# Performance work log

Hardware: AMD Instinct MI355X
Metric: run time of the kernel (lower is better)

## Reference

```python
import jax, jax.numpy as jnp
import numpy as np

jax.config.update("jax_enable_x64", True)  # faithful int64 fixed-point requantize

B, K, N = 2048, 4096, 8192
INT32_MAX_MINUS = 2147418112  # threshold from multiply_by_quantize_mul


def setup_inputs() -> dict:
    key = jax.random.key(0)
    k1, k2, k3 = jax.random.split(key, 3)
    x = jax.random.randint(k1, (B, K), -128, 128, dtype=jnp.int8)
    weights = jax.random.randint(k2, (N, K), -128, 128, dtype=jnp.int8)
    bias = jax.random.randint(k3, (N, 1), -1024, 1024, dtype=jnp.int32)
    return {
        "x": x,
        "weights": weights,
        "bias": bias,
        "q_mantissa": 1431655765,   # ~2/3 in Q31 fixed point
        "exponent": -3,
        "output_zero_point": -5,
    }


def multiply_by_quantize_mul(x, q_mantissa, exponent):
    # Python precedence in original: (q_mantissa + (1<<15)) >> 16
    reduced_mantissa = ((q_mantissa + (1 << 15)) >> 16) if q_mantissa < INT32_MAX_MINUS else 32767
    total_shifts = 15 - exponent
    x = x * np.int64(reduced_mantissa)
    x = x + np.int64(1 << (total_shifts - 1))  # rounding term
    return jnp.right_shift(x, total_shifts)    # arithmetic shift on signed int64


def reference(x, weights, bias, q_mantissa, exponent, output_zero_point):
    # int8 GEMM accumulated in int32: result[b, n] = sum_k x[b, k] * w[n, k]
    acc = jnp.einsum("bk,nk->bn", x.astype(jnp.int32), weights.astype(jnp.int32))
    acc = acc + bias.T  # bias [N,1] -> [1,N], broadcast over batch
    acc = multiply_by_quantize_mul(acc.astype(jnp.int64), q_mantissa, exponent)
    acc = acc + np.int64(output_zero_point)
    out = jnp.clip(acc, -128, 127).astype(jnp.int8)
    return out
```

## Files before the change

kernel.cpp:

```cpp
#include <hip/hip_runtime.h>

#define DEVI __device__ __forceinline__

typedef int i32x4  __attribute__((ext_vector_type(4)));
typedef int i32x16 __attribute__((ext_vector_type(16)));

static constexpr int Bdim = 2048;
static constexpr int Kdim = 4096;
static constexpr int Ndim = 8192;
static constexpr int BK   = 64;
static constexpr int NT   = Kdim / BK;

typedef __attribute__((address_space(1))) const unsigned int gas_t;
typedef __attribute__((address_space(3))) unsigned int las_t;

DEVI void gload_lds16(const void* g, void* l) {
    __builtin_amdgcn_global_load_lds((gas_t*)g, (las_t*)l, 16, 0, 0);
}

DEVI int pack4(i32x4 v) {
    return (v[0] & 255) | ((v[1] & 255) << 8) | ((v[2] & 255) << 16) | (v[3] << 24);
}

__global__ void pack_i32_to_i8(const int* __restrict__ in, char* __restrict__ out, int n16) {
    int i = blockIdx.x * blockDim.x + threadIdx.x;
    if (i >= n16) return;
    const i32x4* src = (const i32x4*)in + (size_t)i * 4;
    i32x4 r;
    r[0] = pack4(src[0]);
    r[1] = pack4(src[1]);
    r[2] = pack4(src[2]);
    r[3] = pack4(src[3]);
    ((i32x4*)out)[i] = r;
}

__global__ __launch_bounds__(512, 4)
void gemm2b(const char* __restrict__ A8, const char* __restrict__ B8,
            const int* __restrict__ bias,
            const int* __restrict__ qm_p, const int* __restrict__ ex_p,
            const int* __restrict__ zp_p, int* __restrict__ out) {
    __shared__ __align__(16) char smem[49152];

    const int tid  = threadIdx.x;
    const int wid  = tid >> 6;
    const int lane = tid & 63;
    const int l31  = lane & 31;
    const int hc   = lane >> 5;
    const int wr   = wid >> 2;
    const int wc   = wid & 3;

    const int bid = blockIdx.x;
    const int swz = (bid & 7) * 64 + (bid >> 3);
    const int bm  = swz >> 5;
    const int bn  = swz & 31;
    const int arow0 = bm * 128;
    const int brow0 = bn * 256;

    const int st_c = (tid & 3) ^ ((tid >> 3) & 3);
    const char* agp = A8 + (size_t)(arow0 + (tid >> 2)) * Kdim + st_c * 16;
    const char* bgp = B8 + (size_t)(brow0 + (tid >> 2)) * Kdim + st_c * 16;

    auto stage = [&](int t) {
        const int buf = (t & 1) * 24576;
        gload_lds16(agp + (size_t)t * BK, &smem[buf + tid * 16]);
        gload_lds16(bgp + (size_t)t * BK, &smem[buf + 8192 + tid * 16]);
        gload_lds16(bgp + (size_t)128 * Kdim + (size_t)t * BK,
                    &smem[buf + 8192 + 8192 + tid * 16]);
    };

    int aoff[2][2], boff[2][2];
#pragma unroll
    for (int m = 0; m < 2; ++m) {
        const int row = wr * 64 + m * 32 + l31;
        const int xr  = (row >> 1) & 3;
#pragma unroll
        for (int s = 0; s < 2; ++s)
            aoff[s][m] = row * 64 + (((s * 2 + hc) ^ xr)) * 16;
    }
#pragma unroll
    for (int n = 0; n < 2; ++n) {
        const int row = wc * 64 + n * 32 + l31;
        const int xr  = (row >> 1) & 3;
#pragma unroll
        for (int s = 0; s < 2; ++s)
            boff[s][n] = 8192 + row * 64 + (((s * 2 + hc) ^ xr)) * 16;
    }

    i32x16 acc[2][2] = {};

    auto compute = [&](int t) {
        const int buf = (t & 1) * 24576;
        i32x4 a[2][2], b[2][2];
#pragma unroll
        for (int s = 0; s < 2; ++s)
#pragma unroll
            for (int m = 0; m < 2; ++m)
                a[s][m] = *(const i32x4*)&smem[buf + aoff[s][m]];
#pragma unroll
        for (int s = 0; s < 2; ++s)
#pragma unroll
            for (int n = 0; n < 2; ++n)
                b[s][n] = *(const i32x4*)&smem[buf + boff[s][n]];
#pragma unroll
        for (int m = 0; m < 2; ++m)
#pragma unroll
            for (int n = 0; n < 2; ++n)
#pragma unroll
                for (int s = 0; s < 2; ++s)
                    acc[m][n] = __builtin_amdgcn_mfma_i32_32x32x32_i8(
                        a[s][m], b[s][n], acc[m][n], 0, 0, 0);
    };

    stage(0);
    __syncthreads();
    for (int t = 0; t < NT; ++t) {
        if (t + 1 < NT) stage(t + 1);
        compute(t);
        __syncthreads();
    }

    const int qm = *qm_p;
    const int ex = *ex_p;
    const int zp = *zp_p;
    const int rm = (qm < 2147418112) ? ((qm + (1 << 15)) >> 16) : 32767;
    const int shifts = 15 - ex;
    const long long rnd = (shifts > 0) ? (1LL << (shifts - 1)) : 0;

    int bv[2];
#pragma unroll
    for (int n = 0; n < 2; ++n) bv[n] = bias[brow0 + wc * 64 + n * 32 + l31];

#pragma unroll
    for (int m = 0; m < 2; ++m) {
        const int rbase = arow0 + wr * 64 + m * 32 + hc * 4;
#pragma unroll
        for (int n = 0; n < 2; ++n) {
            const int col = brow0 + wc * 64 + n * 32 + l31;
#pragma unroll
            for (int j = 0; j < 16; ++j) {
                const int row = rbase + (j & 3) + (j >> 2) * 8;
                long long t = (long long)(acc[m][n][j] + bv[n]) * rm + rnd;
                t >>= shifts;
                t += zp;
                t = t < -128 ? -128 : (t > 127 ? 127 : t);
                out[(size_t)row * Ndim + col] = (int)t;
            }
        }
    }
}

extern "C" void kernel_launch(void* const* d_in, const int* in_sizes, int n_in,
                              void* d_out, int out_size, void* d_ws, size_t ws_size,
                              hipStream_t stream) {
    const int* x32  = (const int*)d_in[0];
    const int* w32  = (const int*)d_in[1];
    const int* bias = (const int*)d_in[2];
    const int* qm   = (const int*)d_in[3];
    const int* ex   = (const int*)d_in[4];
    const int* zp   = (const int*)d_in[5];
    int* out = (int*)d_out;

    char* xa = (char*)d_ws;
    char* wa = xa + (size_t)Bdim * Kdim;
    const int nx16 = Bdim * Kdim / 16;
    const int nw16 = Ndim * Kdim / 16;
    pack_i32_to_i8<<<(nx16 + 255) / 256, 256, 0, stream>>>(x32, xa, nx16);
    pack_i32_to_i8<<<(nw16 + 255) / 256, 256, 0, stream>>>(w32, wa, nw16);

    const int grid = (Bdim / 128) * (Ndim / 256);
    gemm2b<<<grid, 512, 0, stream>>>(xa, wa, bias, qm, ex, zp, out);
}
```

Baseline: 119.5 us.

## Use 256-thread blocks with 64x128 warp tiles and explicit LDS read scheduling

Halves the block to 4 waves while keeping the 128x256 block tile, so each wave now computes a 64x128 sub-tile with 8 accumulators and more MFMA work per LDS fragment loaded. All LDS fragment reads are issued up front with inline ds_read_b128, the next tile's global->LDS prefetch is issued after them, and MFMAs run after an explicit lgkmcnt wait and sched barrier at raised wave priority. This raises register pressure and lowers the number of waves available to hide latency, and the MFMAs no longer overlap with outstanding LDS reads.

```diff
diff --git a/kernel.cpp b/kernel.cpp
--- a/kernel.cpp
+++ b/kernel.cpp
@@ -13,14 +13,26 @@
 
 typedef __attribute__((address_space(1))) const unsigned int gas_t;
 typedef __attribute__((address_space(3))) unsigned int las_t;
+typedef __attribute__((address_space(3))) const char lds_cchar;
 
 DEVI void gload_lds16(const void* g, void* l) {
     __builtin_amdgcn_global_load_lds((gas_t*)g, (las_t*)l, 16, 0, 0);
 }
 
+DEVI i32x4 dsread128(lds_cchar* p) {
+    i32x4 r;
+    asm volatile("ds_read_b128 %0, %1" : "=v"(r) : "v"(p));
+    return r;
+}
+
 DEVI int pack4(i32x4 v) {
     return (v[0] & 255) | ((v[1] & 255) << 8) | ((v[2] & 255) << 16) | (v[3] << 24);
 }
+
+#define WAITLG0 asm volatile("s_waitcnt lgkmcnt(0)" ::: "memory")
+#define SCHB __builtin_amdgcn_sched_barrier(0)
+#define PRIO1 __builtin_amdgcn_s_setprio(1)
+#define PRIO0 __builtin_amdgcn_s_setprio(0)
 
 __global__ void pack_i32_to_i8(const int* __restrict__ in, char* __restrict__ out, int n16) {
     int i = blockIdx.x * blockDim.x + threadIdx.x;
@@ -34,20 +46,21 @@
     ((i32x4*)out)[i] = r;
 }
 
-__global__ __launch_bounds__(512, 4)
-void gemm2b(const char* __restrict__ A8, const char* __restrict__ B8,
-            const int* __restrict__ bias,
-            const int* __restrict__ qm_p, const int* __restrict__ ex_p,
-            const int* __restrict__ zp_p, int* __restrict__ out) {
+__global__ __launch_bounds__(256, 2)
+void gemm9(const char* __restrict__ A8, const char* __restrict__ B8,
+           const int* __restrict__ bias,
+           const int* __restrict__ qm_p, const int* __restrict__ ex_p,
+           const int* __restrict__ zp_p, int* __restrict__ out) {
     __shared__ __align__(16) char smem[49152];
+    lds_cchar* sbase = (lds_cchar*)smem;
 
     const int tid  = threadIdx.x;
     const int wid  = tid >> 6;
     const int lane = tid & 63;
     const int l31  = lane & 31;
     const int hc   = lane >> 5;
-    const int wr   = wid >> 2;
-    const int wc   = wid & 3;
+    const int wr   = wid >> 1;
+    const int wc   = wid & 1;
 
     const int bid = blockIdx.x;
     const int swz = (bid & 7) * 64 + (bid >> 3);
@@ -57,65 +70,63 @@
     const int brow0 = bn * 256;
 
     const int st_c = (tid & 3) ^ ((tid >> 3) & 3);
-    const char* agp = A8 + (size_t)(arow0 + (tid >> 2)) * Kdim + st_c * 16;
-    const char* bgp = B8 + (size_t)(brow0 + (tid >> 2)) * Kdim + st_c * 16;
+    const int r0   = tid >> 2;
+    const char* agp = A8 + (size_t)(arow0 + r0) * Kdim + st_c * 16;
+    const char* bgp = B8 + (size_t)(brow0 + r0) * Kdim + st_c * 16;
 
     auto stage = [&](int t) {
         const int buf = (t & 1) * 24576;
-        gload_lds16(agp + (size_t)t * BK, &smem[buf + tid * 16]);
-        gload_lds16(bgp + (size_t)t * BK, &smem[buf + 8192 + tid * 16]);
-        gload_lds16(bgp + (size_t)128 * Kdim + (size_t)t * BK,
-                    &smem[buf + 8192 + 8192 + tid * 16]);
+        const size_t ko = (size_t)t * BK;
+        gload_lds16(agp + ko,                      &smem[buf + tid * 16]);
+        gload_lds16(agp + ko + (size_t) 64 * Kdim, &smem[buf + tid * 16 + 4096]);
+        gload_lds16(bgp + ko,                      &smem[buf + 8192 + tid * 16]);
+        gload_lds16(bgp + ko + (size_t) 64 * Kdim, &smem[buf + 8192 + tid * 16 + 4096]);
+        gload_lds16(bgp + ko + (size_t)128 * Kdim, &smem[buf + 8192 + tid * 16 + 8192]);
+        gload_lds16(bgp + ko + (size_t)192 * Kdim, &smem[buf + 8192 + tid * 16 + 12288]);
     };
 
-    int aoff[2][2], boff[2][2];
+    const int xr = (l31 >> 1) & 3;
+    int aoff[2][2], boff[2][4];
 #pragma unroll
-    for (int m = 0; m < 2; ++m) {
-        const int row = wr * 64 + m * 32 + l31;
-        const int xr  = (row >> 1) & 3;
+    for (int s = 0; s < 2; ++s) {
+        const int slot16 = ((2 * s + hc) ^ xr) * 16;
 #pragma unroll
-        for (int s = 0; s < 2; ++s)
-            aoff[s][m] = row * 64 + (((s * 2 + hc) ^ xr)) * 16;
-    }
+        for (int m = 0; m < 2; ++m)
+            aoff[s][m] = (wr * 64 + m * 32 + l31) * 64 + slot16;
 #pragma unroll
-    for (int n = 0; n < 2; ++n) {
-        const int row = wc * 64 + n * 32 + l31;
-        const int xr  = (row >> 1) & 3;
-#pragma unroll
-        for (int s = 0; s < 2; ++s)
-            boff[s][n] = 8192 + row * 64 + (((s * 2 + hc) ^ xr)) * 16;
+        for (int n = 0; n < 4; ++n)
+            boff[s][n] = 8192 + (wc * 128 + n * 32 + l31) * 64 + slot16;
     }
 
-    i32x16 acc[2][2] = {};
+    i32x16 acc[2][4] = {};
 
-    auto compute = [&](int t) {
+    stage(0);
+    __syncthreads();
+    for (int t = 0; t < NT; ++t) {
         const int buf = (t & 1) * 24576;
-        i32x4 a[2][2], b[2][2];
+        i32x4 a[2][2], b[2][4];
 #pragma unroll
         for (int s = 0; s < 2; ++s)
 #pragma unroll
             for (int m = 0; m < 2; ++m)
-                a[s][m] = *(const i32x4*)&smem[buf + aoff[s][m]];
+                a[s][m] = dsread128(sbase + (buf + aoff[s][m]));
 #pragma unroll
         for (int s = 0; s < 2; ++s)
 #pragma unroll
-            for (int n = 0; n < 2; ++n)
-                b[s][n] = *(const i32x4*)&smem[buf + boff[s][n]];
+            for (int n = 0; n < 4; ++n)
+                b[s][n] = dsread128(sbase + (buf + boff[s][n]));
+        if (t + 1 < NT) stage(t + 1);
+        WAITLG0; SCHB;
+        PRIO1;
 #pragma unroll
         for (int m = 0; m < 2; ++m)
 #pragma unroll
-            for (int n = 0; n < 2; ++n)
+            for (int n = 0; n < 4; ++n)
 #pragma unroll
                 for (int s = 0; s < 2; ++s)
                     acc[m][n] = __builtin_amdgcn_mfma_i32_32x32x32_i8(
                         a[s][m], b[s][n], acc[m][n], 0, 0, 0);
-    };
-
-    stage(0);
-    __syncthreads();
-    for (int t = 0; t < NT; ++t) {
-        if (t + 1 < NT) stage(t + 1);
-        compute(t);
+        PRIO0;
         __syncthreads();
     }
 
@@ -126,16 +137,16 @@
     const int shifts = 15 - ex;
     const long long rnd = (shifts > 0) ? (1LL << (shifts - 1)) : 0;
 
-    int bv[2];
+    int bv[4];
 #pragma unroll
-    for (int n = 0; n < 2; ++n) bv[n] = bias[brow0 + wc * 64 + n * 32 + l31];
+    for (int n = 0; n < 4; ++n) bv[n] = bias[brow0 + wc * 128 + n * 32 + l31];
 
 #pragma unroll
     for (int m = 0; m < 2; ++m) {
         const int rbase = arow0 + wr * 64 + m * 32 + hc * 4;
 #pragma unroll
-        for (int n = 0; n < 2; ++n) {
-            const int col = brow0 + wc * 64 + n * 32 + l31;
+        for (int n = 0; n < 4; ++n) {
+            const int col = brow0 + wc * 128 + n * 32 + l31;
 #pragma unroll
             for (int j = 0; j < 16; ++j) {
                 const int row = rbase + (j & 3) + (j >> 2) * 8;
@@ -168,5 +179,5 @@
     pack_i32_to_i8<<<(nw16 + 255) / 256, 256, 0, stream>>>(w32, wa, nw16);
 
     const int grid = (Bdim / 128) * (Ndim / 256);
-    gemm2b<<<grid, 512, 0, stream>>>(xa, wa, bias, qm, ex, zp, out);
+    gemm9<<<grid, 256, 0, stream>>>(xa, wa, bias, qm, ex, zp, out);
 }
```

Measured after the change: 119.2 us. No clear change (-0.2%).
